# Optimization experiments

Measured on AMD Instinct MI355X. Metric: run time of the kernel, lower is better.

The kernel has to match this reference:

```python
import jax, jax.numpy as jnp
import numpy as np

N = 512
D = 400          # per-sample feature dim (lstm_hidden_dim * 2)
H = 400          # hidden dim of F_func (lstm_hidden_dim * 2)


def setup_inputs() -> dict:
    key = jax.random.key(0)
    k1, k2, k3, k4, k5, k6 = jax.random.split(key, 6)
    x_samples = jax.random.normal(k1, (N, D), dtype=jnp.float32)
    y_samples = jax.random.normal(k2, (N, D), dtype=jnp.float32)
    # torch nn.Linear default init: U(-1/sqrt(fan_in), 1/sqrt(fan_in))
    b1_bound = 1.0 / np.sqrt(2 * D)
    b2_bound = 1.0 / np.sqrt(H)
    W1 = jax.random.uniform(k3, (H, 2 * D), minval=-b1_bound, maxval=b1_bound, dtype=jnp.float32)
    b1 = jax.random.uniform(k4, (H,), minval=-b1_bound, maxval=b1_bound, dtype=jnp.float32)
    W2 = jax.random.uniform(k5, (1, H), minval=-b2_bound, maxval=b2_bound, dtype=jnp.float32)
    b2 = jax.random.uniform(k6, (1,), minval=-b2_bound, maxval=b2_bound, dtype=jnp.float32)
    return {"x_samples": x_samples, "y_samples": y_samples,
            "W1": W1, "b1": b1, "W2": W2, "b2": b2}


def reference(x_samples, y_samples, W1, b1, W2, b2):
    n = y_samples.shape[0]
    W1x, W1y = W1[:, :D], W1[:, D:]
    hx = x_samples @ W1x.T          # [N, H], contribution of x
    hy = y_samples @ W1y.T          # [N, H], contribution of y

    def score(h):  # second linear + softplus, squeeze out last dim of 1
        return jax.nn.softplus(h @ W2.T + b2)[..., 0]

    # T0[i] = F(x[i], y[i])
    T0 = score(jax.nn.relu(hx + hy + b1))                      # [N]
    # T1[i, j] = F(x[j], y[i])  (x tiled along dim 0, y along dim 1)
    h_pair = jax.nn.relu(hy[:, None, :] + hx[None, :, :] + b1) # [N, N, H]
    T1 = score(h_pair)                                          # [N, N]

    t0_mean = T0.mean()
    lower_bound = t0_mean - (jax.nn.logsumexp(T1, axis=1).mean() - jnp.log(jnp.float32(n)))
    upper_bound = t0_mean - T1.mean()
    return (lower_bound, upper_bound)
```

## Files before the change

### kernel.cpp

```cpp
#include <hip/hip_runtime.h>
#include <math.h>


#define NSAMP 512
#define DIM 400
#define HID 400

__global__ __launch_bounds__(256) void club_gemm_kernel(
    const float* __restrict__ X, const float* __restrict__ Y,
    const float* __restrict__ W1, const float* __restrict__ b1,
    float* __restrict__ hxT0, float* __restrict__ hxT1,
    float* __restrict__ hyb0, float* __restrict__ hyb1)
{
    __shared__ float As[64 * 41];
    __shared__ float Bs[64 * 41];
    const int t  = threadIdx.x;
    const int tx = t & 15;
    const int ty = t >> 4;
    const int n0 = blockIdx.x * 64;
    const int h0 = blockIdx.y * 64;
    const int z  = blockIdx.z;
    const int mat = z >> 1, kh = z & 1;
    const float* __restrict__ src = mat ? Y : X;
    const int wcol0 = (mat ? DIM : 0) + kh * 200;
    const int scol0 = kh * 200;

    float acc[4][4];
#pragma unroll
    for (int c = 0; c < 4; c++)
#pragma unroll
        for (int r = 0; r < 4; r++) acc[c][r] = 0.f;

    for (int kc = 0; kc < 200; kc += 40) {
        __syncthreads();
        for (int idx = t; idx < 640; idx += 256) {
            int n = idx / 10, k4 = idx % 10;
            float4 v = *(const float4*)(src + (size_t)(n0 + n) * DIM + scol0 + kc + 4 * k4);
            float* d = As + n * 41 + 4 * k4;
            d[0] = v.x; d[1] = v.y; d[2] = v.z; d[3] = v.w;
        }
        for (int idx = t; idx < 640; idx += 256) {
            int h = idx / 10, k4 = idx % 10;
            int hrow = h0 + h; if (hrow > HID - 1) hrow = HID - 1;
            float4 v = *(const float4*)(W1 + (size_t)hrow * (2 * DIM) + wcol0 + kc + 4 * k4);
            float* d = Bs + h * 41 + 4 * k4;
            d[0] = v.x; d[1] = v.y; d[2] = v.z; d[3] = v.w;
        }
        __syncthreads();
#pragma unroll 4
        for (int k = 0; k < 40; k++) {
            float a[4], b[4];
#pragma unroll
            for (int r = 0; r < 4; r++) a[r] = As[(4 * ty + r) * 41 + k];
#pragma unroll
            for (int c = 0; c < 4; c++) b[c] = Bs[(4 * tx + c) * 41 + k];
#pragma unroll
            for (int c = 0; c < 4; c++)
#pragma unroll
                for (int r = 0; r < 4; r++)
                    acc[c][r] = fmaf(a[r], b[c], acc[c][r]);
        }
    }

    const bool hvalid = (h0 + 4 * tx) < HID;
    if (mat == 0) {
        float* __restrict__ dst = kh ? hxT1 : hxT0;
        if (hvalid) {
#pragma unroll
            for (int c = 0; c < 4; c++) {
                int h = h0 + 4 * tx + c;
                *(float4*)(dst + (size_t)h * NSAMP + n0 + 4 * ty) =
                    make_float4(acc[c][0], acc[c][1], acc[c][2], acc[c][3]);
            }
        }
    } else {
        float* __restrict__ dst = kh ? hyb1 : hyb0;
        if (hvalid) {
            if (kh == 0) {
                float4 bv = *(const float4*)(b1 + h0 + 4 * tx);
#pragma unroll
                for (int r = 0; r < 4; r++) {
                    acc[0][r] += bv.x; acc[1][r] += bv.y;
                    acc[2][r] += bv.z; acc[3][r] += bv.w;
                }
            }
#pragma unroll
            for (int r = 0; r < 4; r++) {
                int n = n0 + 4 * ty + r;
                *(float4*)(dst + (size_t)n * HID + h0 + 4 * tx) =
                    make_float4(acc[0][r], acc[1][r], acc[2][r], acc[3][r]);
            }
        }
    }
}

__global__ __launch_bounds__(256) void club_pair_kernel(
    const float* __restrict__ hxT0, const float* __restrict__ hxT1,
    const float* __restrict__ hyb0, const float* __restrict__ hyb1,
    const float* __restrict__ W2, const float* __restrict__ b2,
    double* __restrict__ expsum, double* __restrict__ tsum,
    double* __restrict__ diagT)
{
    __shared__ float As[32 * 102];
    __shared__ float Bs[100 * 32];
    __shared__ float W2s[100];
    const int t  = threadIdx.x;
    const int tx = t & 15;
    const int ty = t >> 4;
    const int i0 = blockIdx.x * 32;
    const int j0 = blockIdx.y * 32;

    float acc[2][2] = {{0.f, 0.f}, {0.f, 0.f}};

    for (int hc = 0; hc < HID; hc += 100) {
        __syncthreads();
        for (int idx = t; idx < 800; idx += 256) {
            int i = idx / 25, q = idx % 25;
            size_t off = (size_t)(i0 + i) * HID + hc + 4 * q;
            float4 v0 = *(const float4*)(hyb0 + off);
            float4 v1 = *(const float4*)(hyb1 + off);
            float* d = As + i * 102 + 4 * q;
            d[0] = v0.x + v1.x; d[1] = v0.y + v1.y; d[2] = v0.z + v1.z; d[3] = v0.w + v1.w;
        }
        for (int idx = t; idx < 800; idx += 256) {
            int h = idx >> 3, q = idx & 7;
            size_t off = (size_t)(hc + h) * NSAMP + j0 + 4 * q;
            float4 v0 = *(const float4*)(hxT0 + off);
            float4 v1 = *(const float4*)(hxT1 + off);
            *(float4*)(Bs + h * 32 + 4 * q) =
                make_float4(v0.x + v1.x, v0.y + v1.y, v0.z + v1.z, v0.w + v1.w);
        }
        if (t < 100) W2s[t] = W2[hc + t];
        __syncthreads();
#pragma unroll 4
        for (int h = 0; h < 100; h++) {
            float w  = W2s[h];
            float a0 = As[(2 * ty + 0) * 102 + h];
            float a1 = As[(2 * ty + 1) * 102 + h];
            float2 bv = *(const float2*)(Bs + h * 32 + 2 * tx);
            acc[0][0] = fmaf(fmaxf(a0 + bv.x, 0.f), w, acc[0][0]);
            acc[0][1] = fmaf(fmaxf(a0 + bv.y, 0.f), w, acc[0][1]);
            acc[1][0] = fmaf(fmaxf(a1 + bv.x, 0.f), w, acc[1][0]);
            acc[1][1] = fmaf(fmaxf(a1 + bv.y, 0.f), w, acc[1][1]);
        }
    }

    const float bb2 = b2[0];
#pragma unroll
    for (int r = 0; r < 2; r++) {
        const int i = i0 + 2 * ty + r;
        double eD = 0.0, tD = 0.0;
#pragma unroll
        for (int c = 0; c < 2; c++) {
            const int j = j0 + 2 * tx + c;
            float s  = acc[r][c] + bb2;
            float es = expf(s);
            float T  = log1pf(es);
            eD += 1.0 + (double)es;
            tD += (double)T;
            if (i == j) diagT[i] = (double)T;
        }
        for (int off = 1; off < 16; off <<= 1) {
            eD += __shfl_down(eD, off);
            tD += __shfl_down(tD, off);
        }
        if (tx == 0) {
            expsum[i * 16 + blockIdx.y] = eD;
            tsum  [i * 16 + blockIdx.y] = tD;
        }
    }
}

__global__ __launch_bounds__(512) void club_final_kernel(
    const double* __restrict__ expsum, const double* __restrict__ tsum,
    const double* __restrict__ diagT, float* __restrict__ out)
{
    __shared__ double sh[3 * 512];
    const int t = threadIdx.x;
    double es = 0.0, ts = 0.0;
#pragma unroll
    for (int b = 0; b < 16; b++) { es += expsum[t * 16 + b]; ts += tsum[t * 16 + b]; }
    sh[t] = log(es); sh[512 + t] = ts; sh[1024 + t] = diagT[t];
    __syncthreads();
    for (int off = 256; off > 0; off >>= 1) {
        if (t < off) {
            sh[t]        += sh[t + off];
            sh[512 + t]  += sh[512 + t + off];
            sh[1024 + t] += sh[1024 + t + off];
        }
        __syncthreads();
    }
    if (t == 0) {
        double t0m  = sh[1024] / 512.0;
        double lsem = sh[0]    / 512.0;
        double t1m  = sh[512]  / (512.0 * 512.0);
        out[0] = (float)(t0m - (lsem - log(512.0)));
        out[1] = (float)(t0m - t1m);
    }
}

extern "C" void kernel_launch(void* const* d_in, const int* in_sizes, int n_in,
                              void* d_out, int out_size, void* d_ws, size_t ws_size,
                              hipStream_t stream) {
    const float* X  = (const float*)d_in[0];
    const float* Y  = (const float*)d_in[1];
    const float* W1 = (const float*)d_in[2];
    const float* b1 = (const float*)d_in[3];
    const float* W2 = (const float*)d_in[4];
    const float* b2 = (const float*)d_in[5];
    float* out = (float*)d_out;

    char* ws = (char*)d_ws;
    float*  hxT0   = (float*) (ws);
    float*  hxT1   = (float*) (ws +  819200);
    float*  hyb0   = (float*) (ws + 1638400);
    float*  hyb1   = (float*) (ws + 2457600);
    double* expsum = (double*)(ws + 3276800);
    double* tsum   = (double*)(ws + 3342336);
    double* diagT  = (double*)(ws + 3407872);

    club_gemm_kernel <<<dim3(8, 7, 4),  256, 0, stream>>>(X, Y, W1, b1, hxT0, hxT1, hyb0, hyb1);
    club_pair_kernel <<<dim3(16, 16),   256, 0, stream>>>(hxT0, hxT1, hyb0, hyb1, W2, b2,
                                                          expsum, tsum, diagT);
    club_final_kernel<<<1, 512, 0, stream>>>(expsum, tsum, diagT, out);
}
```

Before: 124.2 us.

## Retile GEMM and pair kernels with smaller per-thread tiles and more blocks

The projection GEMM now uses 512 threads with 2x4 outputs each and 100-wide K chunks. The pair kernel uses 16-row tiles, so its grid doubles, with one j column per thread, 200-wide H chunks and W2 read straight from global memory. The aim is more blocks and waves to fill the GPU and fewer synchronisation rounds. The cost is less register reuse per FMA and more shared-memory loads per flop.

```diff
diff --git a/kernel.cpp b/kernel.cpp
--- a/kernel.cpp
+++ b/kernel.cpp
@@ -6,14 +6,14 @@
 #define DIM 400
 #define HID 400
 
-__global__ __launch_bounds__(256) void club_gemm_kernel(
+__global__ __launch_bounds__(512) void club_gemm_kernel(
     const float* __restrict__ X, const float* __restrict__ Y,
     const float* __restrict__ W1, const float* __restrict__ b1,
     float* __restrict__ hxT0, float* __restrict__ hxT1,
     float* __restrict__ hyb0, float* __restrict__ hyb1)
 {
-    __shared__ float As[64 * 41];
-    __shared__ float Bs[64 * 41];
+    __shared__ float As[64 * 105];
+    __shared__ float Bs[64 * 105];
     const int t  = threadIdx.x;
     const int tx = t & 15;
     const int ty = t >> 4;
@@ -25,68 +25,60 @@
     const int wcol0 = (mat ? DIM : 0) + kh * 200;
     const int scol0 = kh * 200;
 
-    float acc[4][4];
-#pragma unroll
-    for (int c = 0; c < 4; c++)
-#pragma unroll
-        for (int r = 0; r < 4; r++) acc[c][r] = 0.f;
-
-    for (int kc = 0; kc < 200; kc += 40) {
-        __syncthreads();
-        for (int idx = t; idx < 640; idx += 256) {
-            int n = idx / 10, k4 = idx % 10;
+    float acc[4][2];
+#pragma unroll
+    for (int c = 0; c < 4; c++) { acc[c][0] = 0.f; acc[c][1] = 0.f; }
+
+    for (int kc = 0; kc < 200; kc += 100) {
+        __syncthreads();
+        for (int idx = t; idx < 1600; idx += 512) {
+            int n = idx / 25, k4 = idx % 25;
             float4 v = *(const float4*)(src + (size_t)(n0 + n) * DIM + scol0 + kc + 4 * k4);
-            float* d = As + n * 41 + 4 * k4;
+            float* d = As + n * 105 + 4 * k4;
             d[0] = v.x; d[1] = v.y; d[2] = v.z; d[3] = v.w;
         }
-        for (int idx = t; idx < 640; idx += 256) {
-            int h = idx / 10, k4 = idx % 10;
+        for (int idx = t; idx < 1600; idx += 512) {
+            int h = idx / 25, k4 = idx % 25;
             int hrow = h0 + h; if (hrow > HID - 1) hrow = HID - 1;
             float4 v = *(const float4*)(W1 + (size_t)hrow * (2 * DIM) + wcol0 + kc + 4 * k4);
-            float* d = Bs + h * 41 + 4 * k4;
+            float* d = Bs + h * 105 + 4 * k4;
             d[0] = v.x; d[1] = v.y; d[2] = v.z; d[3] = v.w;
         }
         __syncthreads();
 #pragma unroll 4
-        for (int k = 0; k < 40; k++) {
-            float a[4], b[4];
-#pragma unroll
-            for (int r = 0; r < 4; r++) a[r] = As[(4 * ty + r) * 41 + k];
-#pragma unroll
-            for (int c = 0; c < 4; c++) b[c] = Bs[(4 * tx + c) * 41 + k];
-#pragma unroll
-            for (int c = 0; c < 4; c++)
-#pragma unroll
-                for (int r = 0; r < 4; r++)
-                    acc[c][r] = fmaf(a[r], b[c], acc[c][r]);
-        }
-    }
-
-    const bool hvalid = (h0 + 4 * tx) < HID;
-    if (mat == 0) {
-        float* __restrict__ dst = kh ? hxT1 : hxT0;
-        if (hvalid) {
+        for (int k = 0; k < 100; k++) {
+            float a0 = As[(2 * ty + 0) * 105 + k];
+            float a1 = As[(2 * ty + 1) * 105 + k];
+#pragma unroll
+            for (int c = 0; c < 4; c++) {
+                float b = Bs[(4 * tx + c) * 105 + k];
+                acc[c][0] = fmaf(a0, b, acc[c][0]);
+                acc[c][1] = fmaf(a1, b, acc[c][1]);
+            }
+        }
+    }
+
+    if ((h0 + 4 * tx) < HID) {
+        if (mat == 0) {
+            float* __restrict__ dst = kh ? hxT1 : hxT0;
 #pragma unroll
             for (int c = 0; c < 4; c++) {
                 int h = h0 + 4 * tx + c;
-                *(float4*)(dst + (size_t)h * NSAMP + n0 + 4 * ty) =
-                    make_float4(acc[c][0], acc[c][1], acc[c][2], acc[c][3]);
-            }
-        }
-    } else {
-        float* __restrict__ dst = kh ? hyb1 : hyb0;
-        if (hvalid) {
+                *(float2*)(dst + (size_t)h * NSAMP + n0 + 2 * ty) =
+                    make_float2(acc[c][0], acc[c][1]);
+            }
+        } else {
+            float* __restrict__ dst = kh ? hyb1 : hyb0;
             if (kh == 0) {
                 float4 bv = *(const float4*)(b1 + h0 + 4 * tx);
-#pragma unroll
-                for (int r = 0; r < 4; r++) {
-                    acc[0][r] += bv.x; acc[1][r] += bv.y;
-                    acc[2][r] += bv.z; acc[3][r] += bv.w;
-                }
-            }
-#pragma unroll
-            for (int r = 0; r < 4; r++) {
-                int n = n0 + 4 * ty + r;
+                acc[0][0] += bv.x; acc[0][1] += bv.x;
+                acc[1][0] += bv.y; acc[1][1] += bv.y;
+                acc[2][0] += bv.z; acc[2][1] += bv.z;
+                acc[3][0] += bv.w; acc[3][1] += bv.w;
+            }
+#pragma unroll
+            for (int r = 0; r < 2; r++) {
+                int n = n0 + 2 * ty + r;
                 *(float4*)(dst + (size_t)n * HID + h0 + 4 * tx) =
                     make_float4(acc[0][r], acc[1][r], acc[2][r], acc[3][r]);
             }
@@ -101,28 +93,28 @@
     double* __restrict__ expsum, double* __restrict__ tsum,
     double* __restrict__ diagT)
 {
-    __shared__ float As[32 * 102];
-    __shared__ float Bs[100 * 32];
-    __shared__ float W2s[100];
+    __shared__ float As[16 * 204];
+    __shared__ float Bs[200 * 32];
     const int t  = threadIdx.x;
-    const int tx = t & 15;
-    const int ty = t >> 4;
-    const int i0 = blockIdx.x * 32;
+    const int tx = t & 31;
+    const int ty = t >> 5;
+    const int i0 = blockIdx.x * 16;
     const int j0 = blockIdx.y * 32;
-
-    float acc[2][2] = {{0.f, 0.f}, {0.f, 0.f}};
-
-    for (int hc = 0; hc < HID; hc += 100) {
+    const int j  = j0 + tx;
+
+    float acc[2] = {0.f, 0.f};
+
+    for (int hc = 0; hc < HID; hc += 200) {
         __syncthreads();
         for (int idx = t; idx < 800; idx += 256) {
-            int i = idx / 25, q = idx % 25;
+            int i = idx / 50, q = idx % 50;
             size_t off = (size_t)(i0 + i) * HID + hc + 4 * q;
             float4 v0 = *(const float4*)(hyb0 + off);
             float4 v1 = *(const float4*)(hyb1 + off);
-            float* d = As + i * 102 + 4 * q;
-            d[0] = v0.x + v1.x; d[1] = v0.y + v1.y; d[2] = v0.z + v1.z; d[3] = v0.w + v1.w;
-        }
-        for (int idx = t; idx < 800; idx += 256) {
+            *(float4*)(As + i * 204 + 4 * q) =
+                make_float4(v0.x + v1.x, v0.y + v1.y, v0.z + v1.z, v0.w + v1.w);
+        }
+        for (int idx = t; idx < 1600; idx += 256) {
             int h = idx >> 3, q = idx & 7;
             size_t off = (size_t)(hc + h) * NSAMP + j0 + 4 * q;
             float4 v0 = *(const float4*)(hxT0 + off);
@@ -130,18 +122,16 @@
             *(float4*)(Bs + h * 32 + 4 * q) =
                 make_float4(v0.x + v1.x, v0.y + v1.y, v0.z + v1.z, v0.w + v1.w);
         }
-        if (t < 100) W2s[t] = W2[hc + t];
-        __syncthreads();
-#pragma unroll 4
-        for (int h = 0; h < 100; h++) {
-            float w  = W2s[h];
-            float a0 = As[(2 * ty + 0) * 102 + h];
-            float a1 = As[(2 * ty + 1) * 102 + h];
-            float2 bv = *(const float2*)(Bs + h * 32 + 2 * tx);
-            acc[0][0] = fmaf(fmaxf(a0 + bv.x, 0.f), w, acc[0][0]);
-            acc[0][1] = fmaf(fmaxf(a0 + bv.y, 0.f), w, acc[0][1]);
-            acc[1][0] = fmaf(fmaxf(a1 + bv.x, 0.f), w, acc[1][0]);
-            acc[1][1] = fmaf(fmaxf(a1 + bv.y, 0.f), w, acc[1][1]);
+        __syncthreads();
+        const float* __restrict__ w2p = W2 + hc;
+#pragma unroll 8
+        for (int h = 0; h < 200; h++) {
+            float w  = w2p[h];
+            float b  = Bs[h * 32 + tx];
+            float a0 = As[(2 * ty + 0) * 204 + h];
+            float a1 = As[(2 * ty + 1) * 204 + h];
+            acc[0] = fmaf(fmaxf(a0 + b, 0.f), w, acc[0]);
+            acc[1] = fmaf(fmaxf(a1 + b, 0.f), w, acc[1]);
         }
     }
 
@@ -149,18 +139,13 @@
 #pragma unroll
     for (int r = 0; r < 2; r++) {
         const int i = i0 + 2 * ty + r;
-        double eD = 0.0, tD = 0.0;
-#pragma unroll
-        for (int c = 0; c < 2; c++) {
-            const int j = j0 + 2 * tx + c;
-            float s  = acc[r][c] + bb2;
-            float es = expf(s);
-            float T  = log1pf(es);
-            eD += 1.0 + (double)es;
-            tD += (double)T;
-            if (i == j) diagT[i] = (double)T;
-        }
-        for (int off = 1; off < 16; off <<= 1) {
+        float s  = acc[r] + bb2;
+        float es = expf(s);
+        float T  = log1pf(es);
+        if (j == i) diagT[i] = (double)T;
+        double eD = 1.0 + (double)es;
+        double tD = (double)T;
+        for (int off = 16; off > 0; off >>= 1) {
             eD += __shfl_down(eD, off);
             tD += __shfl_down(tD, off);
         }
@@ -219,8 +204,8 @@
     double* tsum   = (double*)(ws + 3342336);
     double* diagT  = (double*)(ws + 3407872);
 
-    club_gemm_kernel <<<dim3(8, 7, 4),  256, 0, stream>>>(X, Y, W1, b1, hxT0, hxT1, hyb0, hyb1);
-    club_pair_kernel <<<dim3(16, 16),   256, 0, stream>>>(hxT0, hxT1, hyb0, hyb1, W2, b2,
-                                                          expsum, tsum, diagT);
+    club_gemm_kernel <<<dim3(8, 7, 4), 512, 0, stream>>>(X, Y, W1, b1, hxT0, hxT1, hyb0, hyb1);
+    club_pair_kernel <<<dim3(32, 16),  256, 0, stream>>>(hxT0, hxT1, hyb0, hyb1, W2, b2,
+                                                         expsum, tsum, diagT);
     club_final_kernel<<<1, 512, 0, stream>>>(expsum, tsum, diagT, out);
 }
```

Result: faster. 115.3 us (-7.1%).
